# Performance work log

Measured on AMD Instinct MI355X. Metric: run time of the kernel, lower is better.

The kernel has to match this reference:

```python
import jax, jax.numpy as jnp
import numpy as np

N = 50257   # vocab size
D = 128     # embedding_dim
B = 2048    # batch
C = 10      # context window size


def setup_inputs() -> dict:
    key = jax.random.key(0)
    ks = jax.random.split(key, 16)
    s = 0.02
    return {
        "x_batch": jax.random.randint(ks[0], (B,), 0, N),
        "context_words_batch": jax.random.randint(ks[1], (B, C), 0, N),
        "eps": jax.random.normal(ks[2], (B, D), dtype=jnp.float32),
        # learned parameters
        "inf_emb": jax.random.normal(ks[3], (N, D), dtype=jnp.float32) * s,
        "W_aff": jax.random.normal(ks[4], (D, 2 * D), dtype=jnp.float32) * s,
        "b_aff": jnp.zeros((D,), dtype=jnp.float32),
        "W_mu": jax.random.normal(ks[5], (D, D), dtype=jnp.float32) * s,
        "b_mu": jnp.zeros((D,), dtype=jnp.float32),
        "W_sig": jax.random.normal(ks[6], (D, D), dtype=jnp.float32) * s,
        "b_sig": jnp.zeros((D,), dtype=jnp.float32),
        "gen_sigma_emb": jax.random.normal(ks[7], (N, D), dtype=jnp.float32) * s,
        "W_gen": jax.random.normal(ks[8], (N, D), dtype=jnp.float32) * s,
        "b_gen": jnp.zeros((N,), dtype=jnp.float32),
    }


def reference(x_batch, context_words_batch, eps, inf_emb, W_aff, b_aff,
              W_mu, b_mu, W_sig, b_sig, gen_sigma_emb, W_gen, b_gen):
    # ---- inference network (vectorized over batch and context) ----
    center = inf_emb[x_batch]                    # [B, D]
    ctx = inf_emb[context_words_batch]           # [B, C, D]
    center_rep = jnp.broadcast_to(center[:, None, :], ctx.shape)  # [B, C, D]
    cat = jnp.concatenate([center_rep, ctx], axis=-1)             # [B, C, 2D]
    h = jax.nn.relu(jnp.einsum("bce,de->bcd", cat, W_aff) + b_aff)
    h_sum = h.sum(axis=1)                        # [B, D]
    inf_mu = h_sum @ W_mu.T + b_mu               # [B, D]
    inf_sigma = jax.nn.softplus(h_sum @ W_sig.T + b_sig)

    # ---- reparameterized sample ----
    z = inf_mu + eps * inf_sigma                 # [B, D]

    # ---- generative / reconstruction term ----
    logits = z @ W_gen.T + b_gen                 # [B, N] (dominant intermediate)
    logp = jax.nn.log_softmax(logits, axis=-1)
    recon = jnp.take_along_axis(logp, context_words_batch, axis=1).sum(-1)  # [B]

    # ---- KL term (faithful to original, incl. use of generative sigma) ----
    sigma = jax.nn.softplus(gen_sigma_emb[x_batch])  # [B, D]
    kl = (jnp.log(sigma / inf_sigma)
          + (inf_sigma ** 2 + (inf_mu - sigma) ** 2) / (2.0 * sigma ** 2)
          - 0.5).sum(-1)                        # [B]

    return (kl - recon).mean()
```

## Files before the change

### kernel.cpp

```cpp
#include <hip/hip_runtime.h>
#include <float.h>
#include <math.h>

#define NV 50257
#define D 128
#define B 2048
#define C 10

#define NVPAD 50272
#define NTILES (NVPAD / 16)
#define NSTREAM 128
#define NG4 (NVPAD * D / 4)
#define LOG2E 1.44269504088896f
#define SC1 0x7F7F7F7F

typedef __attribute__((ext_vector_type(8))) short short8;
typedef __attribute__((ext_vector_type(8))) int int8v;
typedef __attribute__((ext_vector_type(4))) float float4v;

__device__ __forceinline__ float softplus_f(float x) {
    return fmaxf(x, 0.f) + log1pf(expf(-fabsf(x)));
}

__device__ __forceinline__ short f2bf(float f) {
    unsigned u = __float_as_uint(f);
    unsigned r = (u + 0x7FFFu + ((u >> 16) & 1u)) >> 16;
    return (short)r;
}

__global__ __launch_bounds__(256) void k_pre(
    const float* __restrict__ waff, const float* __restrict__ wmu,
    const float* __restrict__ wsig, const float* __restrict__ b_gen,
    short* __restrict__ waff_o, short* __restrict__ wmu_o,
    short* __restrict__ wsig_o, float* __restrict__ bg2, float* __restrict__ out)
{
    const int j = blockIdx.x * 256 + threadIdx.x;
    if (j == 0) out[0] = 0.f;
    if (j < 16384) {
        const float4* src; short4* dst; int jj;
        if (j < 8192)       { src = (const float4*)waff; dst = (short4*)waff_o; jj = j; }
        else if (j < 12288) { src = (const float4*)wmu;  dst = (short4*)wmu_o;  jj = j - 8192; }
        else                { src = (const float4*)wsig; dst = (short4*)wsig_o; jj = j - 12288; }
        const float4 g = src[jj];
        short4 o;
        o.x = f2bf(g.x); o.y = f2bf(g.y); o.z = f2bf(g.z); o.w = f2bf(g.w);
        dst[jj] = o;
    } else {
        const int jj = j - 16384;
        if (jj < NVPAD / 4) {
            const int e0 = jj * 4;
            float4 o;
            o.x = (e0 + 0 < NV) ? b_gen[e0 + 0] * LOG2E : -INFINITY;
            o.y = (e0 + 1 < NV) ? b_gen[e0 + 1] * LOG2E : -INFINITY;
            o.z = (e0 + 2 < NV) ? b_gen[e0 + 2] * LOG2E : -INFINITY;
            o.w = (e0 + 3 < NV) ? b_gen[e0 + 3] * LOG2E : -INFINITY;
            ((float4*)bg2)[jj] = o;
        }
    }
}

#define CONVB 629
__global__ __launch_bounds__(640) void k_main(
    const int* __restrict__ x_batch, const int* __restrict__ ctxw,
    const float* __restrict__ eps, const float* __restrict__ inf_emb,
    const short* __restrict__ waff_bf, const float* __restrict__ b_aff,
    const short* __restrict__ wmu_bf, const float* __restrict__ b_mu,
    const short* __restrict__ wsig_bf, const float* __restrict__ b_sig,
    const float* __restrict__ gen_sig_emb, const float* __restrict__ wg,
    unsigned char* __restrict__ w8,
    float* __restrict__ z_out, unsigned char* __restrict__ z8_out,
    float* __restrict__ kl_out)
{
    const int bid = blockIdx.x;
    const int t = threadIdx.x;

    __shared__ float us[16][132];
    __shared__ float hsp[10][16][132];
    __shared__ float kl_s[8][16];

    if (bid >= 128) {
        const int base = (bid - 128) * (640 * 4) + t;
        #pragma unroll
        for (int k = 0; k < 4; ++k) {
            const int i4 = base + k * 640;
            if (i4 < NG4) {
                const int e0 = i4 * 4;
                int pk = 0;
                if (e0 < NV * D) {
                    const float4 g = ((const float4*)wg)[i4];
                    pk = __builtin_amdgcn_cvt_pk_fp8_f32(g.x, g.y, 0, false);
                    pk = __builtin_amdgcn_cvt_pk_fp8_f32(g.z, g.w, pk, true);
                }
                ((int*)w8)[i4] = pk;
            }
        }
        return;
    }

    const int b0 = bid * 16;
    const int wv = t >> 6;
    const int lane = t & 63;
    const int col16 = lane & 15;
    const int quad = lane >> 4;
    const int brow = b0 + col16;

    const int widx = ctxw[brow * C + wv];
    short8 cx[4];
    #pragma unroll
    for (int ks = 0; ks < 4; ++ks) {
        const float* p = inf_emb + (size_t)widx * D + ks * 32 + quad * 8;
        const float4 g0 = *(const float4*)p;
        const float4 g1 = *(const float4*)(p + 4);
        short8 v;
        v[0] = f2bf(g0.x); v[1] = f2bf(g0.y); v[2] = f2bf(g0.z); v[3] = f2bf(g0.w);
        v[4] = f2bf(g1.x); v[5] = f2bf(g1.y); v[6] = f2bf(g1.z); v[7] = f2bf(g1.w);
        cx[ks] = v;
    }

    if (wv < 8) {
        const int cidx = x_batch[brow];
        short8 ce[4];
        #pragma unroll
        for (int ks = 0; ks < 4; ++ks) {
            const float* p = inf_emb + (size_t)cidx * D + ks * 32 + quad * 8;
            const float4 g0 = *(const float4*)p;
            const float4 g1 = *(const float4*)(p + 4);
            short8 v;
            v[0] = f2bf(g0.x); v[1] = f2bf(g0.y); v[2] = f2bf(g0.z); v[3] = f2bf(g0.w);
            v[4] = f2bf(g1.x); v[5] = f2bf(g1.y); v[6] = f2bf(g1.z); v[7] = f2bf(g1.w);
            ce[ks] = v;
        }
        float4v acc = {0.f, 0.f, 0.f, 0.f};
        #pragma unroll
        for (int ks = 0; ks < 4; ++ks) {
            const short8 bw = *(const short8*)(waff_bf + (wv * 16 + col16) * 256 + ks * 32 + quad * 8);
            acc = __builtin_amdgcn_mfma_f32_16x16x32_bf16(ce[ks], bw, acc, 0, 0, 0);
        }
        #pragma unroll
        for (int r = 0; r < 4; ++r)
            us[quad * 4 + r][wv * 16 + col16] = acc[r];
    }
    __syncthreads();

    float ba[8];
    #pragma unroll
    for (int dt = 0; dt < 8; ++dt) ba[dt] = b_aff[dt * 16 + col16];

    #pragma unroll
    for (int dt = 0; dt < 8; ++dt) {
        float4v a = {0.f, 0.f, 0.f, 0.f};
        #pragma unroll
        for (int ks = 0; ks < 4; ++ks) {
            const short8 bw = *(const short8*)(waff_bf + (dt * 16 + col16) * 256 + 128 + ks * 32 + quad * 8);
            a = __builtin_amdgcn_mfma_f32_16x16x32_bf16(cx[ks], bw, a, 0, 0, 0);
        }
        #pragma unroll
        for (int r = 0; r < 4; ++r) {
            const float u = us[quad * 4 + r][dt * 16 + col16];
            hsp[wv][quad * 4 + r][dt * 16 + col16] = fmaxf(u + a[r] + ba[dt], 0.f);
        }
    }
    __syncthreads();

    if (wv < 8) {
        short8 ha[4];
        #pragma unroll
        for (int ks = 0; ks < 4; ++ks) {
            const int off = ks * 32 + quad * 8;
            float4 s0 = {0.f, 0.f, 0.f, 0.f}, s1 = {0.f, 0.f, 0.f, 0.f};
            #pragma unroll
            for (int w = 0; w < 10; ++w) {
                const float4 a0 = *(const float4*)&hsp[w][col16][off];
                const float4 a1 = *(const float4*)&hsp[w][col16][off + 4];
                s0.x += a0.x; s0.y += a0.y; s0.z += a0.z; s0.w += a0.w;
                s1.x += a1.x; s1.y += a1.y; s1.z += a1.z; s1.w += a1.w;
            }
            short8 v;
            v[0] = f2bf(s0.x); v[1] = f2bf(s0.y); v[2] = f2bf(s0.z); v[3] = f2bf(s0.w);
            v[4] = f2bf(s1.x); v[5] = f2bf(s1.y); v[6] = f2bf(s1.z); v[7] = f2bf(s1.w);
            ha[ks] = v;
        }

        int xb2[4];
        #pragma unroll
        for (int r = 0; r < 4; ++r) xb2[r] = x_batch[b0 + quad * 4 + r];

        const int nt = wv;
        float4v mu4 = {0.f, 0.f, 0.f, 0.f};
        float4v sg4 = {0.f, 0.f, 0.f, 0.f};
        #pragma unroll
        for (int ks = 0; ks < 4; ++ks) {
            const short8 bm = *(const short8*)(wmu_bf + (nt * 16 + col16) * 128 + ks * 32 + quad * 8);
            const short8 bs = *(const short8*)(wsig_bf + (nt * 16 + col16) * 128 + ks * 32 + quad * 8);
            mu4 = __builtin_amdgcn_mfma_f32_16x16x32_bf16(ha[ks], bm, mu4, 0, 0, 0);
            sg4 = __builtin_amdgcn_mfma_f32_16x16x32_bf16(ha[ks], bs, sg4, 0, 0, 0);
        }
        const int d = nt * 16 + col16;
        const float bmu = b_mu[d];
        const float bsg = b_sig[d];
        float klp[4];
        #pragma unroll
        for (int r = 0; r < 4; ++r) {
            const int b = b0 + quad * 4 + r;
            const float mu = mu4[r] + bmu;
            const float sg = sg4[r] + bsg;
            const float isig = softplus_f(sg);
            const float e = eps[b * D + d];
            const float zz = fmaf(e, isig, mu);
            z_out[b * D + d] = zz;
            const int pk = __builtin_amdgcn_cvt_pk_fp8_f32(zz * LOG2E, 0.f, 0, false);
            z8_out[b * D + d] = (unsigned char)(pk & 0xFF);
            const float gs = softplus_f(gen_sig_emb[(size_t)xb2[r] * D + d]);
            const float diff = mu - gs;
            klp[r] = logf(gs / isig) + (isig * isig + diff * diff) / (2.f * gs * gs) - 0.5f;
        }
        #pragma unroll
        for (int off = 1; off < 16; off <<= 1)
            #pragma unroll
            for (int r = 0; r < 4; ++r)
                klp[r] += __shfl_xor(klp[r], off, 64);
        if (col16 == 0) {
            #pragma unroll
            for (int r = 0; r < 4; ++r)
                kl_s[wv][quad * 4 + r] = klp[r];
        }
    }
    __syncthreads();
    if (t < 16) {
        float s = 0.f;
        #pragma unroll
        for (int w = 0; w < 8; ++w) s += kl_s[w][t];
        kl_out[b0 + t] = s;
    }
}

#define LOADT8(bf, g, T) { \
    const int v_ = (T) < NTILES; \
    const int tt_ = v_ ? (T) : 0; \
    bf = *(const int8v*)(w8 + (size_t)(tt_ * 16 + col16) * D + quad * 32); \
    g = v_ ? bg2t[tt_ * 16 + col16] : -INFINITY; }

#define COMP8(bf, g) { \
    _Pragma("unroll") \
    for (int rt = 0; rt < 4; ++rt) { \
        float4v c = {g, g, g, g}; \
        c = __builtin_amdgcn_mfma_scale_f32_16x16x128_f8f6f4( \
                afrag[rt], bf, c, 0, 0, 0, SC1, 0, SC1); \
        _Pragma("unroll") \
        for (int r = 0; r < 4; ++r) \
            sums[rt][r] += __builtin_amdgcn_exp2f(c[r]); \
    } }

__global__ __launch_bounds__(256) void k_lse_mfma(
    const unsigned char* __restrict__ z8, const unsigned char* __restrict__ w8,
    const float* __restrict__ bg2t, float* __restrict__ part_s)
{
    const int bid = blockIdx.x;
    const int s = bid & 127;
    const int x = bid >> 7;
    const int t = threadIdx.x;
    const int wv = t >> 6;
    const int lane = t & 63;
    const int col16 = lane & 15;
    const int quad = lane >> 4;
    const int rowbase = x * 256 + wv * 64;

    int8v afrag[4];
    #pragma unroll
    for (int rt = 0; rt < 4; ++rt)
        afrag[rt] = *(const int8v*)(z8 + (size_t)(rowbase + rt * 16 + col16) * D + quad * 32);

    float sums[4][4];
    #pragma unroll
    for (int rt = 0; rt < 4; ++rt)
        #pragma unroll
        for (int r = 0; r < 4; ++r) sums[rt][r] = 0.f;

    int8v bA, bB, bC, bD;
    float gA, gB, gC, gD;
    LOADT8(bA, gA, s);
    LOADT8(bB, gB, s + 128);
    LOADT8(bC, gC, s + 256);
    LOADT8(bD, gD, s + 384);
    #pragma unroll 1
    for (int j = 0; j < 24; j += 4) {
        COMP8(bA, gA); LOADT8(bA, gA, s + (j + 4) * 128);
        COMP8(bB, gB); LOADT8(bB, gB, s + (j + 5) * 128);
        COMP8(bC, gC); LOADT8(bC, gC, s + (j + 6) * 128);
        COMP8(bD, gD); LOADT8(bD, gD, s + (j + 7) * 128);
    }
    COMP8(bA, gA); COMP8(bB, gB); COMP8(bC, gC); COMP8(bD, gD);

    #pragma unroll
    for (int off = 1; off < 16; off <<= 1)
        #pragma unroll
        for (int rt = 0; rt < 4; ++rt)
            #pragma unroll
            for (int r = 0; r < 4; ++r)
                sums[rt][r] += __shfl_xor(sums[rt][r], off, 64);

    if (col16 == 0) {
        #pragma unroll
        for (int rt = 0; rt < 4; ++rt)
            #pragma unroll
            for (int r = 0; r < 4; ++r) {
                const int row = rowbase + rt * 16 + quad * 4 + r;
                part_s[row * NSTREAM + s] = sums[rt][r];
            }
    }
}

__global__ __launch_bounds__(256) void k_final(
    const float* __restrict__ z, const float* __restrict__ W_gen,
    const float* __restrict__ b_gen, const int* __restrict__ ctxw,
    const float* __restrict__ part_s, const float* __restrict__ kl,
    float* __restrict__ out)
{
    const int t = threadIdx.x;
    const int wv = t >> 6;
    const int lane = t & 63;
    __shared__ float red[4];

    float wsum = 0.f;
    #pragma unroll
    for (int rr = 0; rr < 2; ++rr) {
        const int b = blockIdx.x * 8 + wv * 2 + rr;

        int idxs[C];
        #pragma unroll
        for (int c = 0; c < C; ++c) idxs[c] = ctxw[b * C + c];
        float2 wv2[C];
        #pragma unroll
        for (int c = 0; c < C; ++c)
            wv2[c] = *(const float2*)(W_gen + (size_t)idxs[c] * D + lane * 2);
        float sum_bg = 0.f;
        #pragma unroll
        for (int c = 0; c < C; ++c) sum_bg += b_gen[idxs[c]];

        float sv = part_s[b * NSTREAM + lane] + part_s[b * NSTREAM + 64 + lane];
        const float z0 = z[b * D + lane * 2];
        const float z1 = z[b * D + lane * 2 + 1];

        float acc = 0.f;
        #pragma unroll
        for (int c = 0; c < C; ++c) {
            acc = fmaf(z0, wv2[c].x, acc);
            acc = fmaf(z1, wv2[c].y, acc);
        }
        #pragma unroll
        for (int off = 32; off > 0; off >>= 1) {
            sv  += __shfl_xor(sv, off, 64);
            acc += __shfl_xor(acc, off, 64);
        }
        if (lane == 0) {
            const float lse = logf(sv);
            const float recon = acc + sum_bg - C * lse;
            wsum += kl[b] - recon;
        }
    }
    if (lane == 0) red[wv] = wsum;
    __syncthreads();
    if (t == 0) atomicAdd(out, (red[0] + red[1] + red[2] + red[3]) * (1.f / B));
}

extern "C" void kernel_launch(void* const* d_in, const int* in_sizes, int n_in,
                              void* d_out, int out_size, void* d_ws, size_t ws_size,
                              hipStream_t stream) {
    const int* x_batch = (const int*)d_in[0];
    const int* ctxw    = (const int*)d_in[1];
    const float* eps   = (const float*)d_in[2];
    const float* inf_emb = (const float*)d_in[3];
    const float* W_aff = (const float*)d_in[4];
    const float* b_aff = (const float*)d_in[5];
    const float* W_mu  = (const float*)d_in[6];
    const float* b_mu  = (const float*)d_in[7];
    const float* W_sig = (const float*)d_in[8];
    const float* b_sig = (const float*)d_in[9];
    const float* gen_sig = (const float*)d_in[10];
    const float* W_gen = (const float*)d_in[11];
    const float* b_gen = (const float*)d_in[12];
    float* out = (float*)d_out;

    char* ws = (char*)d_ws;
    float* z      = (float*)ws;   ws += (size_t)B * D * 4;
    float* part_s = (float*)ws;   ws += (size_t)B * NSTREAM * 4;
    float* kl     = (float*)ws;   ws += (size_t)B * 4;
    float* bg2    = (float*)ws;   ws += (size_t)NVPAD * 4;
    unsigned char* z8 = (unsigned char*)ws;  ws += (size_t)B * D;
    unsigned char* w8 = (unsigned char*)ws;  ws += (size_t)NVPAD * D;
    short* waff_bf = (short*)ws;  ws += (size_t)128 * 256 * 2;
    short* wmu_bf  = (short*)ws;  ws += (size_t)128 * 128 * 2;
    short* wsig_bf = (short*)ws;  ws += (size_t)128 * 128 * 2;

    const int pre_items = 16384 + NVPAD / 4;
    hipLaunchKernelGGL(k_pre, dim3((pre_items + 255) / 256), dim3(256), 0, stream,
                       W_aff, W_mu, W_sig, b_gen,
                       waff_bf, wmu_bf, wsig_bf, bg2, out);
    hipLaunchKernelGGL(k_main, dim3(128 + CONVB), dim3(640), 0, stream,
                       x_batch, ctxw, eps, inf_emb, waff_bf, b_aff, wmu_bf, b_mu,
                       wsig_bf, b_sig, gen_sig, W_gen, w8, z, z8, kl);
    hipLaunchKernelGGL(k_lse_mfma, dim3(8 * NSTREAM), dim3(256), 0, stream,
                       z8, w8, bg2, part_s);
    hipLaunchKernelGGL(k_final, dim3(B / 8), dim3(256), 0, stream,
                       z, W_gen, b_gen, ctxw, part_s, kl, out);
}
```

Baseline: 183.5 us.

## Halve LDS partials, trim LSE tail tiles, use fp8 weights in final gather

The per-context ReLU outputs are now summed in pairs through a two-phase LDS write, which halves the hsp shared buffer and the later reduction loop. In exchange it adds one extra barrier and a read-modify-write pass. The LSE streaming loop is shortened, and its tail now loads one extra tile, so the tile count per stream drops from 28 to 25. The final gather reads the fp8-converted W_gen instead of fp32, which cuts gather bandwidth but reduces the precision of the target logit dot products.

Result: faster. 177.2 us (-3.4%).

```diff
diff --git a/kernel.cpp b/kernel.cpp
--- a/kernel.cpp
+++ b/kernel.cpp
@@ -17,6 +17,7 @@
 typedef __attribute__((ext_vector_type(8))) short short8;
 typedef __attribute__((ext_vector_type(8))) int int8v;
 typedef __attribute__((ext_vector_type(4))) float float4v;
+typedef __attribute__((ext_vector_type(2))) float float2v;
 
 __device__ __forceinline__ float softplus_f(float x) {
     return fmaxf(x, 0.f) + log1pf(expf(-fabsf(x)));
@@ -75,7 +76,7 @@
     const int t = threadIdx.x;
 
     __shared__ float us[16][132];
-    __shared__ float hsp[10][16][132];
+    __shared__ float hsp[5][16][132];
     __shared__ float kl_s[8][16];
 
     if (bid >= 128) {
@@ -146,6 +147,7 @@
     #pragma unroll
     for (int dt = 0; dt < 8; ++dt) ba[dt] = b_aff[dt * 16 + col16];
 
+    float4v H[8];
     #pragma unroll
     for (int dt = 0; dt < 8; ++dt) {
         float4v a = {0.f, 0.f, 0.f, 0.f};
@@ -157,8 +159,24 @@
         #pragma unroll
         for (int r = 0; r < 4; ++r) {
             const float u = us[quad * 4 + r][dt * 16 + col16];
-            hsp[wv][quad * 4 + r][dt * 16 + col16] = fmaxf(u + a[r] + ba[dt], 0.f);
-        }
+            H[dt][r] = fmaxf(u + a[r] + ba[dt], 0.f);
+        }
+    }
+
+    if (wv < 5) {
+        #pragma unroll
+        for (int dt = 0; dt < 8; ++dt)
+            #pragma unroll
+            for (int r = 0; r < 4; ++r)
+                hsp[wv][quad * 4 + r][dt * 16 + col16] = H[dt][r];
+    }
+    __syncthreads();
+    if (wv >= 5) {
+        #pragma unroll
+        for (int dt = 0; dt < 8; ++dt)
+            #pragma unroll
+            for (int r = 0; r < 4; ++r)
+                hsp[wv - 5][quad * 4 + r][dt * 16 + col16] += H[dt][r];
     }
     __syncthreads();
 
@@ -169,7 +187,7 @@
             const int off = ks * 32 + quad * 8;
             float4 s0 = {0.f, 0.f, 0.f, 0.f}, s1 = {0.f, 0.f, 0.f, 0.f};
             #pragma unroll
-            for (int w = 0; w < 10; ++w) {
+            for (int w = 0; w < 5; ++w) {
                 const float4 a0 = *(const float4*)&hsp[w][col16][off];
                 const float4 a1 = *(const float4*)&hsp[w][col16][off + 4];
                 s0.x += a0.x; s0.y += a0.y; s0.z += a0.z; s0.w += a0.w;
@@ -283,13 +301,16 @@
     LOADT8(bC, gC, s + 256);
     LOADT8(bD, gD, s + 384);
     #pragma unroll 1
-    for (int j = 0; j < 24; j += 4) {
+    for (int j = 0; j < 20; j += 4) {
         COMP8(bA, gA); LOADT8(bA, gA, s + (j + 4) * 128);
         COMP8(bB, gB); LOADT8(bB, gB, s + (j + 5) * 128);
         COMP8(bC, gC); LOADT8(bC, gC, s + (j + 6) * 128);
         COMP8(bD, gD); LOADT8(bD, gD, s + (j + 7) * 128);
     }
-    COMP8(bA, gA); COMP8(bB, gB); COMP8(bC, gC); COMP8(bD, gD);
+    COMP8(bA, gA);
+    COMP8(bB, gB); COMP8(bC, gC); COMP8(bD, gD);
+    LOADT8(bA, gA, s + 24 * 128);
+    COMP8(bA, gA);
 
     #pragma unroll
     for (int off = 1; off < 16; off <<= 1)
@@ -311,7 +332,7 @@
 }
 
 __global__ __launch_bounds__(256) void k_final(
-    const float* __restrict__ z, const float* __restrict__ W_gen,
+    const float* __restrict__ z, const unsigned char* __restrict__ w8,
     const float* __restrict__ b_gen, const int* __restrict__ ctxw,
     const float* __restrict__ part_s, const float* __restrict__ kl,
     float* __restrict__ out)
@@ -329,10 +350,10 @@
         int idxs[C];
         #pragma unroll
         for (int c = 0; c < C; ++c) idxs[c] = ctxw[b * C + c];
-        float2 wv2[C];
+        unsigned short uw[C];
         #pragma unroll
         for (int c = 0; c < C; ++c)
-            wv2[c] = *(const float2*)(W_gen + (size_t)idxs[c] * D + lane * 2);
+            uw[c] = *(const unsigned short*)(w8 + (size_t)idxs[c] * D + lane * 2);
         float sum_bg = 0.f;
         #pragma unroll
         for (int c = 0; c < C; ++c) sum_bg += b_gen[idxs[c]];
@@ -344,8 +365,9 @@
         float acc = 0.f;
         #pragma unroll
         for (int c = 0; c < C; ++c) {
-            acc = fmaf(z0, wv2[c].x, acc);
-            acc = fmaf(z1, wv2[c].y, acc);
+            const float2v wf = __builtin_amdgcn_cvt_pk_f32_fp8((int)uw[c], false);
+            acc = fmaf(z0, wf[0], acc);
+            acc = fmaf(z1, wf[1], acc);
         }
         #pragma unroll
         for (int off = 32; off > 0; off >>= 1) {
@@ -402,5 +424,5 @@
     hipLaunchKernelGGL(k_lse_mfma, dim3(8 * NSTREAM), dim3(256), 0, stream,
                        z8, w8, bg2, part_s);
     hipLaunchKernelGGL(k_final, dim3(B / 8), dim3(256), 0, stream,
-                       z, W_gen, b_gen, ctxw, part_s, kl, out);
-}
+                       z, w8, b_gen, ctxw, part_s, kl, out);
+}
```
